# Kernel optimization log

Measured on AMD Instinct MI355X. Metric: run time of the kernel, lower is better.

Reference implementation:

```python
import jax, jax.numpy as jnp
import numpy as np

N_NODES = 131072
N_EDGES = 1048576
N_GRAPHS = 1024
EMB = 96
HID = 64
OUT = 3
NEG_SLOPE = 0.2  # PyG GATConv default leaky_relu slope


def setup_inputs() -> dict:
    key = jax.random.key(0)
    ks = jax.random.split(key, 8)
    x = jax.random.normal(ks[0], (N_NODES, EMB), dtype=jnp.float32)
    edge_index = jax.random.randint(ks[1], (2, N_EDGES), 0, N_NODES, dtype=jnp.int64)
    batch = jnp.sort(jax.random.randint(ks[2], (N_NODES,), 0, N_GRAPHS, dtype=jnp.int64))
    s = 1.0 / np.sqrt(EMB)
    W = jax.random.uniform(ks[3], (EMB, HID), jnp.float32, -s, s)       # GATConv lin (no bias)
    att_src = jax.random.uniform(ks[4], (HID,), jnp.float32, -s, s)     # a_src
    att_dst = jax.random.uniform(ks[5], (HID,), jnp.float32, -s, s)     # a_dst
    bias_gat = jnp.zeros((HID,), jnp.float32)
    sf = 1.0 / np.sqrt(HID)
    fc_w = jax.random.uniform(ks[6], (OUT, HID), jnp.float32, -sf, sf)
    fc_b = jax.random.uniform(ks[7], (OUT,), jnp.float32, -sf, sf)
    return {"x": x, "edge_index": edge_index, "batch": batch, "W": W,
            "att_src": att_src, "att_dst": att_dst, "bias_gat": bias_gat,
            "fc_w": fc_w, "fc_b": fc_b}


def _segment_softmax(logits, seg, num_segments):
    # numerically stable softmax over edges grouped by target node
    m = jax.ops.segment_max(logits, seg, num_segments=num_segments)
    e = jnp.exp(logits - m[seg])
    z = jax.ops.segment_sum(e, seg, num_segments=num_segments)
    return e / (z[seg] + 1e-16)


def reference(x, edge_index, batch, W, att_src, att_dst, bias_gat, fc_w, fc_b):
    N = x.shape[0]
    # PyG GATConv (heads=1): add self loops
    loop = jnp.arange(N, dtype=edge_index.dtype)
    src = jnp.concatenate([edge_index[0], loop])
    dst = jnp.concatenate([edge_index[1], loop])

    h = x @ W                                    # [N, HID]
    a_s = h @ att_src                            # [N]
    a_d = h @ att_dst                            # [N]
    logits = jax.nn.leaky_relu(a_s[src] + a_d[dst], NEG_SLOPE)  # [E]
    alpha = _segment_softmax(logits, dst, N)     # softmax over in-edges per target
    out = jax.ops.segment_sum(alpha[:, None] * h[src], dst, num_segments=N)
    out = out + bias_gat                         # [N, HID]

    # global_mean_pool over graphs
    sums = jax.ops.segment_sum(out, batch, num_segments=N_GRAPHS)
    cnt = jax.ops.segment_sum(jnp.ones((N,), out.dtype), batch, num_segments=N_GRAPHS)
    pooled = sums / jnp.maximum(cnt, 1.0)[:, None]  # [G, HID]

    logits_out = pooled @ fc_w.T + fc_b          # [G, OUT]
    return jax.nn.log_softmax(logits_out, axis=1)
```

## Files before the change

kernel.cpp:

```cpp
#include <hip/hip_runtime.h>
#include <hip/hip_fp16.h>

#define N_NODES 131072
#define N_EDGES 1048576
#define N_GRAPHS 1024
#define EMB 96
#define HID 64
#define OUT 3
#define CAP 32
#define NBKT 512
#define NCHUNK 256
#define BCAP 32
#define LCAP 16

typedef _Float16 half8 __attribute__((ext_vector_type(8)));
typedef float float4v __attribute__((ext_vector_type(4)));

__global__ __launch_bounds__(512, 4) void k_front(
    const int* __restrict__ src, const int* __restrict__ dst,
    int* __restrict__ ebuf, int* __restrict__ ccnt,
    const float* __restrict__ x, const float* __restrict__ W,
    const float* __restrict__ att_src, const float* __restrict__ att_dst,
    __half* __restrict__ h, float* __restrict__ a_s, float* __restrict__ a_d,
    float* __restrict__ poolz)
{
    int tid = threadIdx.x;
    __shared__ int smem[NBKT * LCAP + NBKT];

    if (blockIdx.x < NCHUNK) {
        int blk = blockIdx.x;
        int* lists16 = smem;
        int* bcnt = smem + NBKT * LCAP;
        bcnt[tid] = 0;
        if (blk < 33) {
            int idx = blk * 512 + tid;
            if (idx < (N_GRAPHS * HID + N_GRAPHS) / 4)
                ((float4*)poolz)[idx] = (float4){0.f, 0.f, 0.f, 0.f};
        }
        __syncthreads();
        int e0 = blk * 4096;
        #pragma unroll
        for (int i = 0; i < 8; ++i) {
            int e = e0 + i * 512 + tid;
            int sv = src[e], dv = dst[e];
            int b = dv >> 8;
            int packed = (sv << 8) | (dv & 255);
            int r = atomicAdd(&bcnt[b], 1);
            if (r < LCAP)
                lists16[b * LCAP + r] = packed;
            else if (r < BCAP)
                ebuf[((size_t)blk * NBKT + b) * BCAP + r] = packed;
        }
        __syncthreads();
        #pragma unroll
        for (int it = 0; it < 16; ++it) {
            int idx = it * 512 + tid;
            int seg = idx >> 4, s = idx & 15;
            ebuf[((size_t)blk * NBKT + seg) * BCAP + s] = lists16[idx];
        }
        int v = bcnt[tid];
        ccnt[blk * NBKT + tid] = v < BCAP ? v : BCAP;
    } else {
        int sub = blockIdx.x - NCHUNK;
        _Float16* lwt = (_Float16*)smem;
        #pragma unroll
        for (int i = 0; i < 12; ++i) {
            int idx = i * 512 + tid;
            lwt[(idx & 63) * 104 + (idx >> 6)] = (_Float16)W[idx];
        }
        __syncthreads();

        int lane = tid & 63;
        int w = tid >> 6;
        int m16 = lane & 15;
        int quad = lane >> 4;
        int rowbase = sub * 128 + w * 16;

        half8 bf[4][3];
        #pragma unroll
        for (int nt = 0; nt < 4; ++nt)
            #pragma unroll
            for (int kb = 0; kb < 3; ++kb)
                bf[nt][kb] = *(const half8*)(lwt + (nt * 16 + m16) * 104
                                             + kb * 32 + quad * 8);

        float4v acc[4];
        #pragma unroll
        for (int nt = 0; nt < 4; ++nt)
            acc[nt] = (float4v){0.f, 0.f, 0.f, 0.f};

        const float* xrow = x + (size_t)(rowbase + m16) * EMB + quad * 8;
        #pragma unroll
        for (int kb = 0; kb < 3; ++kb) {
            float4 xa = *(const float4*)(xrow + kb * 32);
            float4 xb = *(const float4*)(xrow + kb * 32 + 4);
            half8 af;
            af[0] = (_Float16)xa.x; af[1] = (_Float16)xa.y;
            af[2] = (_Float16)xa.z; af[3] = (_Float16)xa.w;
            af[4] = (_Float16)xb.x; af[5] = (_Float16)xb.y;
            af[6] = (_Float16)xb.z; af[7] = (_Float16)xb.w;
            #pragma unroll
            for (int nt = 0; nt < 4; ++nt)
                acc[nt] = __builtin_amdgcn_mfma_f32_16x16x32_f16(
                    af, bf[nt][kb], acc[nt], 0, 0, 0);
        }

        float asv[4], adv[4];
        #pragma unroll
        for (int nt = 0; nt < 4; ++nt) {
            asv[nt] = att_src[nt * 16 + m16];
            adv[nt] = att_dst[nt * 16 + m16];
        }

        #pragma unroll
        for (int r = 0; r < 4; ++r) {
            int row = rowbase + quad * 4 + r;
            float ps = 0.f, pd = 0.f;
            #pragma unroll
            for (int nt = 0; nt < 4; ++nt) {
                float v = acc[nt][r];
                h[(size_t)row * HID + nt * 16 + m16] = __float2half(v);
                ps += v * asv[nt];
                pd += v * adv[nt];
            }
            #pragma unroll
            for (int off = 8; off >= 1; off >>= 1) {
                ps += __shfl_xor(ps, off, 64);
                pd += __shfl_xor(pd, off, 64);
            }
            if (m16 == 0) { a_s[row] = ps; a_d[row] = pd; }
        }
    }
}

__global__ __launch_bounds__(512, 2) void k_place_accum(
    const int* __restrict__ ebuf, const int* __restrict__ ccnt,
    const __half2* __restrict__ h2, const float* __restrict__ a_s,
    const float* __restrict__ a_d, const float* __restrict__ bias,
    __half2* __restrict__ out)
{
    int tid = threadIdx.x;
    int b = blockIdx.x;
    __shared__ int lists[256 * CAP];
    __shared__ int cl[256];
    __shared__ int cm[NCHUNK];
    __shared__ float wbuf[32 * CAP];
    if (tid < 256) cl[tid] = 0;
    if (tid < NCHUNK) cm[tid] = ccnt[tid * NBKT + b];
    __syncthreads();

    {
        int e[8];
        #pragma unroll
        for (int k = 0; k < 8; ++k) {
            int c = k * 32 + (tid >> 4);
            e[k] = ebuf[((size_t)c * NBKT + b) * BCAP + (tid & 15)];
        }
        #pragma unroll
        for (int k = 0; k < 8; ++k) {
            int c = k * 32 + (tid >> 4);
            if ((tid & 15) < cm[c]) {
                int local = e[k] & 255;
                int slot = atomicAdd(&cl[local], 1);
                if (slot < CAP)
                    lists[local * CAP + slot] = e[k] >> 8;
            }
        }
    }
    if (tid < NCHUNK) {
        int n = cm[tid];
        for (int s = 16; s < n; ++s) {
            int ev = ebuf[((size_t)tid * NBKT + b) * BCAP + s];
            int local = ev & 255;
            int slot = atomicAdd(&cl[local], 1);
            if (slot < CAP)
                lists[local * CAP + slot] = ev >> 8;
        }
    }
    __syncthreads();

    int lane = tid & 63;
    int sub = lane & 31;
    int gbase = lane & 32;
    int wv = tid >> 6;
    int grp = tid >> 5;
    float2 b2 = ((const float2*)bias)[sub];

    for (int p = 0; p < 16; p += 2) {
        int localA = p * 16 + wv * 2 + (gbase >> 5);
        int localB = localA + 16;
        int nodeA = b * 256 + localA;
        int nodeB = b * 256 + localB;
        int degA = cl[localA]; if (degA > CAP) degA = CAP;
        int degB = cl[localB]; if (degB > CAP) degB = CAP;

        __half2 hvA = h2[(size_t)nodeA * 32 + sub];
        __half2 hvB = h2[(size_t)nodeB * 32 + sub];
        __half2 hgA[16], hgB[16];
        #pragma unroll
        for (int k = 0; k < 16; ++k) {
            int s = lists[localA * CAP + k];
            s = (k < degA) ? s : nodeA;
            hgA[k] = h2[(size_t)s * 32 + sub];
        }
        #pragma unroll
        for (int k = 0; k < 16; ++k) {
            int s = lists[localB * CAP + k];
            s = (k < degB) ? s : nodeB;
            hgB[k] = h2[(size_t)s * 32 + sub];
        }

        int svA = lists[localA * CAP + sub];
        int s_jA = (sub < degA) ? svA : nodeA;
        int svB = lists[localB * CAP + sub];
        int s_jB = (sub < degB) ? svB : nodeB;
        float asgA = a_s[s_jA];
        float asgB = a_s[s_jB];
        float adiA = a_d[nodeA], asiA = a_s[nodeA];
        float adiB = a_d[nodeB], asiB = a_s[nodeB];

        float tA = asgA + adiA; tA = tA > 0.f ? tA : 0.2f * tA;
        float w_jA = (sub < degA) ? __expf(tA) : 0.f;
        wbuf[grp * CAP + sub] = w_jA;
        float tB = asgB + adiB; tB = tB > 0.f ? tB : 0.2f * tB;
        float w_jB = (sub < degB) ? __expf(tB) : 0.f;
        wbuf[(16 + grp) * CAP + sub] = w_jB;

        float t0A = asiA + adiA; t0A = t0A > 0.f ? t0A : 0.2f * t0A;
        float w0A = __expf(t0A);
        float t0B = asiB + adiB; t0B = t0B > 0.f ? t0B : 0.2f * t0B;
        float w0B = __expf(t0B);

        float zA = w_jA, zB = w_jB;
        #pragma unroll
        for (int off = 16; off >= 1; off >>= 1) {
            zA += __shfl_xor(zA, off, 64);
            zB += __shfl_xor(zB, off, 64);
        }
        zA += w0A; zB += w0B;

        float2 accA, accB;
        accA.x = w0A * __half2float(hvA.x);
        accA.y = w0A * __half2float(hvA.y);
        accB.x = w0B * __half2float(hvB.x);
        accB.y = w0B * __half2float(hvB.y);
        #pragma unroll
        for (int k = 0; k < 16; ++k) {
            float wkA = wbuf[grp * CAP + k];
            accA.x += wkA * __half2float(hgA[k].x);
            accA.y += wkA * __half2float(hgA[k].y);
            float wkB = wbuf[(16 + grp) * CAP + k];
            accB.x += wkB * __half2float(hgB[k].x);
            accB.y += wkB * __half2float(hgB[k].y);
        }

        for (int j0 = 16; j0 < degA; j0 += 8) {
            __half2 g2[8];
            #pragma unroll
            for (int k = 0; k < 8; ++k) {
                int s = lists[localA * CAP + j0 + k];
                s = (j0 + k < degA) ? s : nodeA;
                g2[k] = h2[(size_t)s * 32 + sub];
            }
            #pragma unroll
            for (int k = 0; k < 8; ++k) {
                float wk = wbuf[grp * CAP + j0 + k];
                accA.x += wk * __half2float(g2[k].x);
                accA.y += wk * __half2float(g2[k].y);
            }
        }
        for (int j0 = 16; j0 < degB; j0 += 8) {
            __half2 g2[8];
            #pragma unroll
            for (int k = 0; k < 8; ++k) {
                int s = lists[localB * CAP + j0 + k];
                s = (j0 + k < degB) ? s : nodeB;
                g2[k] = h2[(size_t)s * 32 + sub];
            }
            #pragma unroll
            for (int k = 0; k < 8; ++k) {
                float wk = wbuf[(16 + grp) * CAP + j0 + k];
                accB.x += wk * __half2float(g2[k].x);
                accB.y += wk * __half2float(g2[k].y);
            }
        }

        float invA = 1.f / (zA + 1e-16f);
        float invB = 1.f / (zB + 1e-16f);
        out[(size_t)nodeA * 32 + sub] =
            __floats2half2_rn(accA.x * invA + b2.x, accA.y * invA + b2.y);
        out[(size_t)nodeB * 32 + sub] =
            __floats2half2_rn(accB.x * invB + b2.x, accB.y * invB + b2.y);
    }
}

__global__ __launch_bounds__(256) void k_pool(const __half* __restrict__ out,
    const int* __restrict__ batch, float* __restrict__ pool,
    float* __restrict__ gcnt)
{
    int lane = threadIdx.x & 63;
    int wv = blockIdx.x * 4 + (threadIdx.x >> 6);
    int base = wv * 64;
    int bv = batch[base + lane];
    int g_cur = __shfl(bv, 0);
    float acc = 0.f;
    int run = 0;
    for (int c = 0; c < 8; ++c) {
        int n0 = base + c * 8;
        float v[8];
        #pragma unroll
        for (int k = 0; k < 8; ++k)
            v[k] = __half2float(out[(size_t)(n0 + k) * HID + lane]);
        int b0 = __shfl(bv, c * 8);
        int b7 = __shfl(bv, c * 8 + 7);
        if (b0 == b7) {
            if (b0 != g_cur) {
                atomicAdd(&pool[g_cur * HID + lane], acc);
                if (lane == 0) atomicAdd(&gcnt[g_cur], (float)run);
                acc = 0.f; run = 0; g_cur = b0;
            }
            acc += ((v[0] + v[1]) + (v[2] + v[3]))
                 + ((v[4] + v[5]) + (v[6] + v[7]));
            run += 8;
        } else {
            #pragma unroll
            for (int k = 0; k < 8; ++k) {
                int g = __shfl(bv, c * 8 + k);
                if (g != g_cur) {
                    atomicAdd(&pool[g_cur * HID + lane], acc);
                    if (lane == 0) atomicAdd(&gcnt[g_cur], (float)run);
                    acc = 0.f; run = 0; g_cur = g;
                }
                acc += v[k]; ++run;
            }
        }
    }
    atomicAdd(&pool[g_cur * HID + lane], acc);
    if (lane == 0) atomicAdd(&gcnt[g_cur], (float)run);
}

__global__ __launch_bounds__(256) void k_head(const float* __restrict__ pool,
    const float* __restrict__ gcnt, const float* __restrict__ fc_w,
    const float* __restrict__ fc_b, float* __restrict__ out)
{
    int tid = threadIdx.x;
    int lane = tid & 63;
    int g = blockIdx.x * 4 + (tid >> 6);
    float p = pool[g * HID + lane] / fmaxf(gcnt[g], 1.0f);
    float l0 = p * fc_w[0 * HID + lane];
    float l1 = p * fc_w[1 * HID + lane];
    float l2 = p * fc_w[2 * HID + lane];
    #pragma unroll
    for (int off = 32; off >= 1; off >>= 1) {
        l0 += __shfl_xor(l0, off, 64);
        l1 += __shfl_xor(l1, off, 64);
        l2 += __shfl_xor(l2, off, 64);
    }
    l0 += fc_b[0]; l1 += fc_b[1]; l2 += fc_b[2];
    float m = fmaxf(l0, fmaxf(l1, l2));
    float lse = m + logf(__expf(l0 - m) + __expf(l1 - m) + __expf(l2 - m));
    if (lane == 0) {
        out[g * 3 + 0] = l0 - lse;
        out[g * 3 + 1] = l1 - lse;
        out[g * 3 + 2] = l2 - lse;
    }
}

extern "C" void kernel_launch(void* const* d_in, const int* in_sizes, int n_in,
                              void* d_out, int out_size, void* d_ws, size_t ws_size,
                              hipStream_t stream)
{
    const float* x        = (const float*)d_in[0];
    const int*   ei       = (const int*)d_in[1];
    const int*   batch    = (const int*)d_in[2];
    const float* W        = (const float*)d_in[3];
    const float* att_src  = (const float*)d_in[4];
    const float* att_dst  = (const float*)d_in[5];
    const float* bias_gat = (const float*)d_in[6];
    const float* fc_w     = (const float*)d_in[7];
    const float* fc_b     = (const float*)d_in[8];
    float* out = (float*)d_out;

    char* ws = (char*)d_ws;
    size_t off = 0;
    auto alloc = [&](size_t bytes) {
        void* p = ws + off;
        off += (bytes + 255) & ~(size_t)255;
        return p;
    };
    __half* h    = (__half*)alloc((size_t)N_NODES * HID * 2);
    float* pool  = (float*)alloc((size_t)N_GRAPHS * HID * 4);
    float* gcnt  = (float*)alloc((size_t)N_GRAPHS * 4);
    float* a_s   = (float*)alloc((size_t)N_NODES * 4);
    float* a_d   = (float*)alloc((size_t)N_NODES * 4);
    int*   ccnt  = (int*)  alloc((size_t)NCHUNK * NBKT * 4);
    int*   ebuf  = (int*)  alloc((size_t)NCHUNK * NBKT * BCAP * 4);
    __half* nout = (__half*)alloc((size_t)N_NODES * HID * 2);

    const int* e_src = ei;
    const int* e_dst = ei + N_EDGES;

    k_front<<<NCHUNK + 1024, 512, 0, stream>>>(e_src, e_dst, ebuf, ccnt,
                                               x, W, att_src, att_dst,
                                               h, a_s, a_d, pool);
    k_place_accum<<<NBKT, 512, 0, stream>>>(ebuf, ccnt, (const __half2*)h,
                                            a_s, a_d, bias_gat, (__half2*)nout);
    k_pool <<<N_NODES / 256, 256, 0, stream>>>(nout, batch, pool, gcnt);
    k_head <<<N_GRAPHS / 4, 256, 0, stream>>>(pool, gcnt, fc_w, fc_b, out);
}
```

Baseline: 152.8 us.

## Fuse mean-pool accumulation into GAT aggregation kernel, drop intermediate node output

```diff
diff --git a/kernel.cpp b/kernel.cpp
--- a/kernel.cpp
+++ b/kernel.cpp
@@ -137,7 +137,8 @@
     const int* __restrict__ ebuf, const int* __restrict__ ccnt,
     const __half2* __restrict__ h2, const float* __restrict__ a_s,
     const float* __restrict__ a_d, const float* __restrict__ bias,
-    __half2* __restrict__ out)
+    const int* __restrict__ batch, float* __restrict__ pool,
+    float* __restrict__ gcnt)
 {
     int tid = threadIdx.x;
     int b = blockIdx.x;
@@ -186,6 +187,10 @@
     int grp = tid >> 5;
     float2 b2 = ((const float2*)bias)[sub];
 
+    int g_cur = -1;
+    float2 racc; racc.x = 0.f; racc.y = 0.f;
+    float rcnt = 0.f;
+
     for (int p = 0; p < 16; p += 2) {
         int localA = p * 16 + wv * 2 + (gbase >> 5);
         int localB = localA + 16;
@@ -218,6 +223,8 @@
         float asgB = a_s[s_jB];
         float adiA = a_d[nodeA], asiA = a_s[nodeA];
         float adiB = a_d[nodeB], asiB = a_s[nodeB];
+        int gA = batch[nodeA];
+        int gB = batch[nodeB];
 
         float tA = asgA + adiA; tA = tA > 0.f ? tA : 0.2f * tA;
         float w_jA = (sub < degA) ? __expf(tA) : 0.f;
@@ -287,56 +294,36 @@
 
         float invA = 1.f / (zA + 1e-16f);
         float invB = 1.f / (zB + 1e-16f);
-        out[(size_t)nodeA * 32 + sub] =
-            __floats2half2_rn(accA.x * invA + b2.x, accA.y * invA + b2.y);
-        out[(size_t)nodeB * 32 + sub] =
-            __floats2half2_rn(accB.x * invB + b2.x, accB.y * invB + b2.y);
-    }
-}
-
-__global__ __launch_bounds__(256) void k_pool(const __half* __restrict__ out,
-    const int* __restrict__ batch, float* __restrict__ pool,
-    float* __restrict__ gcnt)
-{
-    int lane = threadIdx.x & 63;
-    int wv = blockIdx.x * 4 + (threadIdx.x >> 6);
-    int base = wv * 64;
-    int bv = batch[base + lane];
-    int g_cur = __shfl(bv, 0);
-    float acc = 0.f;
-    int run = 0;
-    for (int c = 0; c < 8; ++c) {
-        int n0 = base + c * 8;
-        float v[8];
-        #pragma unroll
-        for (int k = 0; k < 8; ++k)
-            v[k] = __half2float(out[(size_t)(n0 + k) * HID + lane]);
-        int b0 = __shfl(bv, c * 8);
-        int b7 = __shfl(bv, c * 8 + 7);
-        if (b0 == b7) {
-            if (b0 != g_cur) {
-                atomicAdd(&pool[g_cur * HID + lane], acc);
-                if (lane == 0) atomicAdd(&gcnt[g_cur], (float)run);
-                acc = 0.f; run = 0; g_cur = b0;
-            }
-            acc += ((v[0] + v[1]) + (v[2] + v[3]))
-                 + ((v[4] + v[5]) + (v[6] + v[7]));
-            run += 8;
-        } else {
-            #pragma unroll
-            for (int k = 0; k < 8; ++k) {
-                int g = __shfl(bv, c * 8 + k);
-                if (g != g_cur) {
-                    atomicAdd(&pool[g_cur * HID + lane], acc);
-                    if (lane == 0) atomicAdd(&gcnt[g_cur], (float)run);
-                    acc = 0.f; run = 0; g_cur = g;
+
+        {
+            __half2 vA = __floats2half2_rn(accA.x * invA + b2.x,
+                                           accA.y * invA + b2.y);
+            if (gA != g_cur) {
+                if (g_cur >= 0) {
+                    atomicAdd(&pool[g_cur * HID + 2 * sub],     racc.x);
+                    atomicAdd(&pool[g_cur * HID + 2 * sub + 1], racc.y);
+                    if (sub == 0) atomicAdd(&gcnt[g_cur], rcnt);
                 }
-                acc += v[k]; ++run;
-            }
-        }
-    }
-    atomicAdd(&pool[g_cur * HID + lane], acc);
-    if (lane == 0) atomicAdd(&gcnt[g_cur], (float)run);
+                g_cur = gA; racc.x = 0.f; racc.y = 0.f; rcnt = 0.f;
+            }
+            racc.x += __half2float(vA.x); racc.y += __half2float(vA.y);
+            rcnt += 1.f;
+
+            __half2 vB = __floats2half2_rn(accB.x * invB + b2.x,
+                                           accB.y * invB + b2.y);
+            if (gB != g_cur) {
+                atomicAdd(&pool[g_cur * HID + 2 * sub],     racc.x);
+                atomicAdd(&pool[g_cur * HID + 2 * sub + 1], racc.y);
+                if (sub == 0) atomicAdd(&gcnt[g_cur], rcnt);
+                g_cur = gB; racc.x = 0.f; racc.y = 0.f; rcnt = 0.f;
+            }
+            racc.x += __half2float(vB.x); racc.y += __half2float(vB.y);
+            rcnt += 1.f;
+        }
+    }
+    atomicAdd(&pool[g_cur * HID + 2 * sub],     racc.x);
+    atomicAdd(&pool[g_cur * HID + 2 * sub + 1], racc.y);
+    if (sub == 0) atomicAdd(&gcnt[g_cur], rcnt);
 }
 
 __global__ __launch_bounds__(256) void k_head(const float* __restrict__ pool,
@@ -395,7 +382,6 @@
     float* a_d   = (float*)alloc((size_t)N_NODES * 4);
     int*   ccnt  = (int*)  alloc((size_t)NCHUNK * NBKT * 4);
     int*   ebuf  = (int*)  alloc((size_t)NCHUNK * NBKT * BCAP * 4);
-    __half* nout = (__half*)alloc((size_t)N_NODES * HID * 2);
 
     const int* e_src = ei;
     const int* e_dst = ei + N_EDGES;
@@ -404,7 +390,7 @@
                                                x, W, att_src, att_dst,
                                                h, a_s, a_d, pool);
     k_place_accum<<<NBKT, 512, 0, stream>>>(ebuf, ccnt, (const __half2*)h,
-                                            a_s, a_d, bias_gat, (__half2*)nout);
-    k_pool <<<N_NODES / 256, 256, 0, stream>>>(nout, batch, pool, gcnt);
+                                            a_s, a_d, bias_gat, batch,
+                                            pool, gcnt);
     k_head <<<N_GRAPHS / 4, 256, 0, stream>>>(pool, gcnt, fc_w, fc_b, out);
 }
```

New measurement: 157.9 us. 1.03x slower.
